# Performance work log

Hardware: AMD Instinct MI355X
Metric: run time of the kernel (lower is better)

Reference implementation:

```python
import jax, jax.numpy as jnp
import numpy as np

NUM_HEADS = 16


def setup_inputs() -> dict:
    key = jax.random.key(0)
    k1, k2, k3 = jax.random.split(key, 3)
    b, d, s = 2, 1024, 2048
    x = jax.random.normal(k1, (b, d, s), dtype=jnp.float32)
    # torch nn.Linear(d, 3d) without bias == x @ W1 with W1 of shape (d, 3d)
    W1 = jax.random.normal(k2, (d, 3 * d), dtype=jnp.float32) * (d ** -0.5)
    W2 = jax.random.normal(k3, (d, d), dtype=jnp.float32) * (d ** -0.5)
    return {"x": x, "W1": W1, "W2": W2}


def reference(x, W1, W2):
    # x: (b, hidden_dim, s) -> (b, s, hidden_dim)
    b, d, s = x.shape
    h = NUM_HEADS
    hd = d // h
    xt = jnp.swapaxes(x, 1, 2)                       # (b, s, d)
    qkv = xt @ W1                                    # (b, s, 3d)
    qkv = qkv.reshape(b, s, 3, h, hd)
    qkv = jnp.transpose(qkv, (2, 0, 3, 1, 4))        # (3, b, h, s, hd)
    q, k, v = qkv[0], qkv[1], qkv[2]
    scale = hd ** -0.5
    scores = jnp.einsum("bhqd,bhkd->bhqk", q, k) * scale  # (b, h, s, s)
    # causal mask: same as torch code (adds float32 min where not lower-tri)
    neg = jnp.finfo(jnp.float32).min
    causal = jnp.tril(jnp.ones((s, s), dtype=bool))
    scores = jnp.where(causal[None, None, :, :], scores, scores + neg)
    attn = jax.nn.softmax(scores, axis=-1)           # dropout = identity (eval)
    out = jnp.einsum("bhqk,bhkd->bhqd", attn, v)     # (b, h, s, hd)
    out = jnp.transpose(out, (0, 2, 1, 3)).reshape(b, s, d)
    out = out @ W2                                   # (b, s, d)
    return jnp.swapaxes(out, 1, 2)                   # (b, d, s)
```

## Files before the change

kernel.cpp:

```cpp
#include <hip/hip_runtime.h>
#include <math.h>

#define B_  2
#define D_  1024
#define S_  2048
#define H_  16
#define HD_ 64
#define D3_ 3072
#define M_  4096

typedef __attribute__((ext_vector_type(8))) short short8;
typedef __attribute__((ext_vector_type(4))) float float4v;

__device__ __forceinline__ short f2bf(float f) {
    unsigned u = __builtin_bit_cast(unsigned, f);
    unsigned r = (u + 0x7FFFu + ((u >> 16) & 1u)) >> 16;
    return (short)r;
}

__device__ __forceinline__ unsigned cvt_pk_bf16(float lo, float hi) {
    unsigned r;
    asm("v_cvt_pk_bf16_f32 %0, %1, %2" : "=v"(r) : "v"(lo), "v"(hi));
    return r;
}

__device__ __forceinline__ float fast_exp2(float x) {
    float r;
    asm("v_exp_f32 %0, %1" : "=v"(r) : "v"(x));
    return r;
}

#define GLD16(gsrc, ldst)                                                      \
    __builtin_amdgcn_global_load_lds(                                          \
        (const __attribute__((address_space(1))) void*)(gsrc),                 \
        (__attribute__((address_space(3))) void*)(ldst), 16, 0, 0)

__global__ __launch_bounds__(256) void transpose_cvt(const float* __restrict__ in,
                                                     short* __restrict__ out,
                                                     int R, int C) {
    __shared__ float t[32][33];
    const int c0 = blockIdx.x * 32, r0 = blockIdx.y * 32;
    const float* inb = in + (size_t)blockIdx.z * R * C;
    short* outb = out + (size_t)blockIdx.z * R * C;
    const int tx = threadIdx.x, ty = threadIdx.y;
    #pragma unroll
    for (int i = ty; i < 32; i += 8)
        t[i][tx] = inb[(size_t)(r0 + i) * C + c0 + tx];
    __syncthreads();
    #pragma unroll
    for (int i = ty; i < 32; i += 8)
        outb[(size_t)(c0 + i) * R + r0 + tx] = f2bf(t[tx][i]);
}

__device__ __forceinline__ void gemm_core(const short* __restrict__ A,
                                          const short* __restrict__ Bt,
                                          int m0, int n0,
                                          short* As, short* Bs,
                                          float4v acc[4][4]) {
    const int tid = threadIdx.x;
    const int lane = tid & 63, w = tid >> 6;
    const int wr = (w >> 1) * 64, wc = (w & 1) * 64;
    const int srow = lane >> 2;
    const int scol = (lane & 3) * 8;
    for (int k0 = 0; k0 < 1024; k0 += 32) {
        #pragma unroll
        for (int j = 0; j < 2; ++j) {
            const int ch = 2 * w + j;
            GLD16(A  + (size_t)(m0 + ch * 16 + srow) * 1024 + k0 + scol,
                  As + ch * 512 + lane * 8);
            GLD16(Bt + (size_t)(n0 + ch * 16 + srow) * 1024 + k0 + scol,
                  Bs + ch * 512 + lane * 8);
        }
        __syncthreads();
        short8 a[4], b[4];
        #pragma unroll
        for (int m = 0; m < 4; ++m)
            a[m] = *(const short8*)&As[(wr + m * 16 + (lane & 15)) * 32 + (lane >> 4) * 8];
        #pragma unroll
        for (int n = 0; n < 4; ++n)
            b[n] = *(const short8*)&Bs[(wc + n * 16 + (lane & 15)) * 32 + (lane >> 4) * 8];
        #pragma unroll
        for (int m = 0; m < 4; ++m)
            #pragma unroll
            for (int n = 0; n < 4; ++n)
                acc[m][n] = __builtin_amdgcn_mfma_f32_16x16x32_bf16(a[m], b[n], acc[m][n], 0, 0, 0);
        __syncthreads();
    }
}

__global__ __launch_bounds__(256) void gemm_qkv_mfma(const short* __restrict__ xt,
                                                     const short* __restrict__ W1t,
                                                     short* __restrict__ q,
                                                     short* __restrict__ kk,
                                                     short* __restrict__ vt) {
    __shared__ short As[128 * 32], Bs[128 * 32];
    float4v acc[4][4];
    #pragma unroll
    for (int m = 0; m < 4; ++m)
        #pragma unroll
        for (int n = 0; n < 4; ++n) acc[m][n] = (float4v){0.f, 0.f, 0.f, 0.f};
    const int m0 = blockIdx.y * 128, n0 = blockIdx.x * 128;
    gemm_core(xt, W1t, m0, n0, As, Bs, acc);
    const int lane = threadIdx.x & 63, w = threadIdx.x >> 6;
    const int wr = (w >> 1) * 64, wc = (w & 1) * 64;
    const float qscale = 0.125f * 1.44269504f;
    #pragma unroll
    for (int n = 0; n < 4; ++n) {
        const int gcol = n0 + wc + n * 16 + (lane & 15);
        const int which = gcol >> 10, hh = (gcol >> 6) & 15, hd = gcol & 63;
        #pragma unroll
        for (int m = 0; m < 4; ++m) {
            #pragma unroll
            for (int ri = 0; ri < 4; ++ri) {
                const int grow = m0 + wr + m * 16 + (lane >> 4) * 4 + ri;
                const int bb = grow >> 11, ss = grow & (S_ - 1);
                float av = acc[m][n][ri];
                if (which == 0) av *= qscale;
                const short v = f2bf(av);
                if (which == 0)      q [((size_t)(bb * H_ + hh) * S_ + ss) * HD_ + hd] = v;
                else if (which == 1) kk[((size_t)(bb * H_ + hh) * S_ + ss) * HD_ + hd] = v;
                else                 vt[((size_t)(bb * H_ + hh) * HD_ + hd) * S_ + ss] = v;
            }
        }
    }
}

__global__ __launch_bounds__(256) void attn_mfma(const short* __restrict__ q,
                                                 const short* __restrict__ k,
                                                 const short* __restrict__ vt,
                                                 short* __restrict__ ao) {
    __shared__ short Ks[2][64 * 64];
    __shared__ short Vts[2][64 * 64];
    __shared__ short Ps[64 * 64];
    __shared__ float sums[64];
    const int tid = threadIdx.x;
    const int lane = tid & 63, w = tid >> 6;
    const int bid = (int)blockIdx.x;
    const int xcd = bid & 7, slot = bid >> 3;
    const int bh = xcd * 4 + (slot & 3);
    const int qpair = slot >> 2;
    const size_t base = (size_t)bh * S_ * HD_;
    const short* qp = q + base;
    const short* kp = k + base;
    const short* vp = vt + base;
    const int bb = bh >> 4, hh = bh & 15;
    const int wrow = w * 16;

    for (int half = 0; half < 2; ++half) {
        const int qt = (half == 0) ? qpair : 31 - qpair;
        const int q0 = qt * 64;
        short8 qf[2];
        #pragma unroll
        for (int ks = 0; ks < 2; ++ks)
            qf[ks] = *(const short8*)&qp[(size_t)(q0 + wrow + (lane & 15)) * HD_
                                         + ks * 32 + (lane >> 4) * 8];
        float4v accO[4];
        float lsum = 0.f;
        #pragma unroll
        for (int n = 0; n < 4; ++n) accO[n] = (float4v){0.f, 0.f, 0.f, 0.f};

        const int nkb = qt + 1;
        __syncthreads();
        #pragma unroll
        for (int j = 0; j < 2; ++j) {
            const int g = (w * 2 + j) * 64 + lane;
            const int r = g >> 3, cs = g & 7;
            const int co = (cs ^ (r & 7)) << 3;
            GLD16(kp + (size_t)r * HD_ + co, &Ks[0][g * 8]);
            GLD16(vp + (size_t)r * S_ + co,  &Vts[0][g * 8]);
        }
        int cur = 0;
        for (int kb = 0; kb < nkb; ++kb) {
            const int kv0 = kb * 64;
            __syncthreads();
            if (kb + 1 < nkb) {
                const int kv1 = kv0 + 64;
                #pragma unroll
                for (int j = 0; j < 2; ++j) {
                    const int g = (w * 2 + j) * 64 + lane;
                    const int r = g >> 3, cs = g & 7;
                    const int co = (cs ^ (r & 7)) << 3;
                    GLD16(kp + (size_t)(kv1 + r) * HD_ + co, &Ks[cur ^ 1][g * 8]);
                    GLD16(vp + (size_t)r * S_ + kv1 + co,    &Vts[cur ^ 1][g * 8]);
                }
            }
            float4v accS[4];
            #pragma unroll
            for (int n = 0; n < 4; ++n) accS[n] = (float4v){0.f, 0.f, 0.f, 0.f};
            #pragma unroll
            for (int ks = 0; ks < 2; ++ks) {
                #pragma unroll
                for (int n = 0; n < 4; ++n) {
                    const int rowk = n * 16 + (lane & 15);
                    const int ch = ks * 4 + (lane >> 4);
                    const short8 kf = *(const short8*)&Ks[cur][rowk * 64 + ((ch ^ (rowk & 7)) << 3)];
                    accS[n] = __builtin_amdgcn_mfma_f32_16x16x32_bf16(kf, qf[ks], accS[n], 0, 0, 0);
                }
            }
            const bool diag = (kb == qt);
            const int qg = q0 + wrow + (lane & 15);
            const int prow = wrow + (lane & 15);
            #pragma unroll
            for (int n = 0; n < 4; ++n) {
                const int kvb = kv0 + n * 16 + ((lane >> 4) << 2);
                float p[4];
                if (diag) {
                    const int dlim = qg - kvb;
                    #pragma unroll
                    for (int ri = 0; ri < 4; ++ri)
                        p[ri] = (ri <= dlim) ? fast_exp2(accS[n][ri]) : 0.f;
                } else {
                    #pragma unroll
                    for (int ri = 0; ri < 4; ++ri)
                        p[ri] = fast_exp2(accS[n][ri]);
                }
                lsum += (p[0] + p[1]) + (p[2] + p[3]);
                const unsigned lo = cvt_pk_bf16(p[0], p[1]);
                const unsigned hi = cvt_pk_bf16(p[2], p[3]);
                const int col = n * 16 + ((lane >> 4) << 2);
                const int ch = col >> 3;
                const int addr = prow * 64 + ((ch ^ (prow & 7)) << 3) + (col & 7);
                *(uint2*)&Ps[addr] = (uint2){lo, hi};
            }
            #pragma unroll
            for (int ks = 0; ks < 2; ++ks) {
                const int prow2 = wrow + (lane & 15);
                const int chp = ks * 4 + (lane >> 4);
                const short8 pf = *(const short8*)&Ps[prow2 * 64 + ((chp ^ (prow2 & 7)) << 3)];
                #pragma unroll
                for (int n = 0; n < 4; ++n) {
                    const int vrow = n * 16 + (lane & 15);
                    const int ch = ks * 4 + (lane >> 4);
                    const short8 vf = *(const short8*)&Vts[cur][vrow * 64 + ((ch ^ (vrow & 7)) << 3)];
                    accO[n] = __builtin_amdgcn_mfma_f32_16x16x32_bf16(pf, vf, accO[n], 0, 0, 0);
                }
            }
            cur ^= 1;
        }
        {
            float t = lsum;
            t += __shfl_xor(t, 16);
            t += __shfl_xor(t, 32);
            if (lane < 16) sums[wrow + lane] = t;
        }
        #pragma unroll
        for (int ri = 0; ri < 4; ++ri) {
            const int lrow = wrow + ((lane >> 4) << 2) + ri;
            const float inv = 1.f / sums[lrow];
            const int grow = q0 + lrow;
            #pragma unroll
            for (int n = 0; n < 4; ++n) {
                const int col = hh * 64 + n * 16 + (lane & 15);
                ao[((size_t)(bb * S_ + grow)) * D_ + col] = f2bf(accO[n][ri] * inv);
            }
        }
    }
}

__global__ __launch_bounds__(256) void gemm_out_mfma(const short* __restrict__ W2t,
                                                     const short* __restrict__ ao,
                                                     float* __restrict__ out) {
    __shared__ short As[128 * 32], Bs[128 * 32];
    float4v acc[4][4];
    #pragma unroll
    for (int m = 0; m < 4; ++m)
        #pragma unroll
        for (int n = 0; n < 4; ++n) acc[m][n] = (float4v){0.f, 0.f, 0.f, 0.f};
    const int m0 = blockIdx.y * 128, n0 = blockIdx.x * 128;
    gemm_core(W2t, ao, m0, n0, As, Bs, acc);
    const int lane = threadIdx.x & 63, w = threadIdx.x >> 6;
    const int wr = (w >> 1) * 64, wc = (w & 1) * 64;
    #pragma unroll
    for (int m = 0; m < 4; ++m) {
        #pragma unroll
        for (int ri = 0; ri < 4; ++ri) {
            const int grow = m0 + wr + m * 16 + (lane >> 4) * 4 + ri;
            #pragma unroll
            for (int n = 0; n < 4; ++n) {
                const int gcol = n0 + wc + n * 16 + (lane & 15);
                const int bb = gcol >> 11, ss = gcol & (S_ - 1);
                out[(size_t)bb * D_ * S_ + (size_t)grow * S_ + ss] = acc[m][n][ri];
            }
        }
    }
}

extern "C" void kernel_launch(void* const* d_in, const int* in_sizes, int n_in,
                              void* d_out, int out_size, void* d_ws, size_t ws_size,
                              hipStream_t stream) {
    const float* x  = (const float*)d_in[0];
    const float* W1 = (const float*)d_in[1];
    const float* W2 = (const float*)d_in[2];
    float* out = (float*)d_out;

    short* xt  = (short*)d_ws;
    short* W1t = xt  + (size_t)M_ * D_;
    short* W2t = W1t + (size_t)D3_ * D_;
    short* q   = W2t + (size_t)D_ * D_;
    short* kk  = q   + (size_t)B_ * H_ * S_ * HD_;
    short* vt  = kk  + (size_t)B_ * H_ * S_ * HD_;
    short* ao  = vt  + (size_t)B_ * H_ * S_ * HD_;

    transpose_cvt<<<dim3(S_ / 32, D_ / 32, B_), dim3(32, 8), 0, stream>>>(x, xt, D_, S_);
    transpose_cvt<<<dim3(D3_ / 32, D_ / 32, 1), dim3(32, 8), 0, stream>>>(W1, W1t, D_, D3_);
    transpose_cvt<<<dim3(D_ / 32, D_ / 32, 1), dim3(32, 8), 0, stream>>>(W2, W2t, D_, D_);
    gemm_qkv_mfma<<<dim3(D3_ / 128, M_ / 128), 256, 0, stream>>>(xt, W1t, q, kk, vt);
    attn_mfma<<<dim3(512), 256, 0, stream>>>(q, kk, vt, ao);
    gemm_out_mfma<<<dim3(M_ / 128, D_ / 128), 256, 0, stream>>>(W2t, ao, out);
}
```

Measured before the change: 121.2 us.

## Double-buffer LDS tiles in MFMA GEMMs to overlap global loads with compute

Splits the GEMM main loop into stage and compute steps and ping-pongs two LDS buffers, so the next K-tile's global_load_lds is issued before the MFMAs on the current tile run. A custom gate (vmcnt(0) wait plus barrier plus sched_barrier) replaces the two __syncthreads per iteration with one per tile. This hides global load latency in both the QKV and output projection GEMMs. In exchange it doubles LDS use per block, which may reduce occupancy.

```diff
diff --git a/kernel.cpp b/kernel.cpp
--- a/kernel.cpp
+++ b/kernel.cpp
@@ -34,6 +34,12 @@
     __builtin_amdgcn_global_load_lds(                                          \
         (const __attribute__((address_space(1))) void*)(gsrc),                 \
         (__attribute__((address_space(3))) void*)(ldst), 16, 0, 0)
+
+__device__ __forceinline__ void gate() {
+    asm volatile("s_waitcnt vmcnt(0)" ::: "memory");
+    __builtin_amdgcn_s_barrier();
+    __builtin_amdgcn_sched_barrier(0);
+}
 
 __global__ __launch_bounds__(256) void transpose_cvt(const float* __restrict__ in,
                                                      short* __restrict__ out,
@@ -52,39 +58,58 @@
         outb[(size_t)(c0 + i) * R + r0 + tx] = f2bf(t[tx][i]);
 }
 
+__device__ __forceinline__ void gemm_stage(const short* __restrict__ A,
+                                           const short* __restrict__ Bt,
+                                           int m0, int n0, int k0,
+                                           short* As, short* Bs,
+                                           int w, int lane) {
+    const int srow = lane >> 2;
+    const int scol = (lane & 3) * 8;
+    #pragma unroll
+    for (int j = 0; j < 2; ++j) {
+        const int ch = 2 * w + j;
+        GLD16(A  + (size_t)(m0 + ch * 16 + srow) * 1024 + k0 + scol,
+              As + ch * 512 + lane * 8);
+        GLD16(Bt + (size_t)(n0 + ch * 16 + srow) * 1024 + k0 + scol,
+              Bs + ch * 512 + lane * 8);
+    }
+}
+
+__device__ __forceinline__ void gemm_compute(const short* As, const short* Bs,
+                                             float4v acc[4][4],
+                                             int lane, int wr, int wc) {
+    short8 a[4], b[4];
+    #pragma unroll
+    for (int m = 0; m < 4; ++m)
+        a[m] = *(const short8*)&As[(wr + m * 16 + (lane & 15)) * 32 + (lane >> 4) * 8];
+    #pragma unroll
+    for (int n = 0; n < 4; ++n)
+        b[n] = *(const short8*)&Bs[(wc + n * 16 + (lane & 15)) * 32 + (lane >> 4) * 8];
+    #pragma unroll
+    for (int m = 0; m < 4; ++m)
+        #pragma unroll
+        for (int n = 0; n < 4; ++n)
+            acc[m][n] = __builtin_amdgcn_mfma_f32_16x16x32_bf16(a[m], b[n], acc[m][n], 0, 0, 0);
+}
+
 __device__ __forceinline__ void gemm_core(const short* __restrict__ A,
                                           const short* __restrict__ Bt,
                                           int m0, int n0,
-                                          short* As, short* Bs,
+                                          short* As0, short* Bs0,
+                                          short* As1, short* Bs1,
                                           float4v acc[4][4]) {
     const int tid = threadIdx.x;
     const int lane = tid & 63, w = tid >> 6;
     const int wr = (w >> 1) * 64, wc = (w & 1) * 64;
-    const int srow = lane >> 2;
-    const int scol = (lane & 3) * 8;
-    for (int k0 = 0; k0 < 1024; k0 += 32) {
-        #pragma unroll
-        for (int j = 0; j < 2; ++j) {
-            const int ch = 2 * w + j;
-            GLD16(A  + (size_t)(m0 + ch * 16 + srow) * 1024 + k0 + scol,
-                  As + ch * 512 + lane * 8);
-            GLD16(Bt + (size_t)(n0 + ch * 16 + srow) * 1024 + k0 + scol,
-                  Bs + ch * 512 + lane * 8);
-        }
-        __syncthreads();
-        short8 a[4], b[4];
-        #pragma unroll
-        for (int m = 0; m < 4; ++m)
-            a[m] = *(const short8*)&As[(wr + m * 16 + (lane & 15)) * 32 + (lane >> 4) * 8];
-        #pragma unroll
-        for (int n = 0; n < 4; ++n)
-            b[n] = *(const short8*)&Bs[(wc + n * 16 + (lane & 15)) * 32 + (lane >> 4) * 8];
-        #pragma unroll
-        for (int m = 0; m < 4; ++m)
-            #pragma unroll
-            for (int n = 0; n < 4; ++n)
-                acc[m][n] = __builtin_amdgcn_mfma_f32_16x16x32_bf16(a[m], b[n], acc[m][n], 0, 0, 0);
-        __syncthreads();
+    gemm_stage(A, Bt, m0, n0, 0, As0, Bs0, w, lane);
+    for (int t = 0; t < 32; t += 2) {
+        gate();
+        gemm_stage(A, Bt, m0, n0, (t + 1) * 32, As1, Bs1, w, lane);
+        gemm_compute(As0, Bs0, acc, lane, wr, wc);
+        gate();
+        if (t + 2 < 32)
+            gemm_stage(A, Bt, m0, n0, (t + 2) * 32, As0, Bs0, w, lane);
+        gemm_compute(As1, Bs1, acc, lane, wr, wc);
     }
 }
 
@@ -93,14 +118,14 @@
                                                      short* __restrict__ q,
                                                      short* __restrict__ kk,
                                                      short* __restrict__ vt) {
-    __shared__ short As[128 * 32], Bs[128 * 32];
+    __shared__ short As[2][128 * 32], Bs[2][128 * 32];
     float4v acc[4][4];
     #pragma unroll
     for (int m = 0; m < 4; ++m)
         #pragma unroll
         for (int n = 0; n < 4; ++n) acc[m][n] = (float4v){0.f, 0.f, 0.f, 0.f};
     const int m0 = blockIdx.y * 128, n0 = blockIdx.x * 128;
-    gemm_core(xt, W1t, m0, n0, As, Bs, acc);
+    gemm_core(xt, W1t, m0, n0, As[0], Bs[0], As[1], Bs[1], acc);
     const int lane = threadIdx.x & 63, w = threadIdx.x >> 6;
     const int wr = (w >> 1) * 64, wc = (w & 1) * 64;
     const float qscale = 0.125f * 1.44269504f;
@@ -260,14 +285,14 @@
 __global__ __launch_bounds__(256) void gemm_out_mfma(const short* __restrict__ W2t,
                                                      const short* __restrict__ ao,
                                                      float* __restrict__ out) {
-    __shared__ short As[128 * 32], Bs[128 * 32];
+    __shared__ short As[2][128 * 32], Bs[2][128 * 32];
     float4v acc[4][4];
     #pragma unroll
     for (int m = 0; m < 4; ++m)
         #pragma unroll
         for (int n = 0; n < 4; ++n) acc[m][n] = (float4v){0.f, 0.f, 0.f, 0.f};
     const int m0 = blockIdx.y * 128, n0 = blockIdx.x * 128;
-    gemm_core(W2t, ao, m0, n0, As, Bs, acc);
+    gemm_core(W2t, ao, m0, n0, As[0], Bs[0], As[1], Bs[1], acc);
     const int lane = threadIdx.x & 63, w = threadIdx.x >> 6;
     const int wr = (w >> 1) * 64, wc = (w & 1) * 64;
     #pragma unroll
```

After: 125.7 us. 1.04x slower.
